# Kernel tuning notes

Hardware: AMD Instinct MI355X
Metric: run time of the kernel (lower is better)

The kernel has to match this reference:

```python
import jax, jax.numpy as jnp
import numpy as np

B, L, DIN = 2, 4096, 1024
W = 64            # windowsize
G, H = 8, 8       # groups, heads per group
DQ = DV = 64
FF = 1024
NEG = -1e30


def rmsnorm(x, gamma, d):
    # F.normalize(x, dim=-1) * sqrt(d) * gamma
    n = jnp.sqrt(jnp.sum(x * x, axis=-1, keepdims=True))
    return x / jnp.maximum(n, 1e-12) * (d ** 0.5) * gamma


def setup_inputs() -> dict:
    key = jax.random.key(0)
    ks = jax.random.split(key, 8)
    s = 0.02
    return {
        "x": jax.random.normal(ks[0], (B, L, DIN), jnp.float32),
        "norm_gamma": jnp.ones((DIN,), jnp.float32),
        "Wq_w": jax.random.normal(ks[1], (G * H * DQ, DIN), jnp.float32) * s,
        "Wq_b": jnp.zeros((G * H * DQ,), jnp.float32),
        "Wkv_w": jax.random.normal(ks[2], (G * (DQ + DV), DIN), jnp.float32) * s,
        "Wkv_b": jnp.zeros((G * (DQ + DV),), jnp.float32),
        "wz_gamma1": jnp.ones((G * H * DV,), jnp.float32),
        "W1_w": jax.random.normal(ks[3], (2 * FF, G * H * DV), jnp.float32) * s,
        "W1_b": jnp.zeros((2 * FF,), jnp.float32),
        "wz_gamma2": jnp.ones((2 * FF,), jnp.float32),
        "W2_w": jax.random.normal(ks[4], (FF, 2 * FF), jnp.float32) * s,
        "W2_b": jnp.zeros((FF,), jnp.float32),
    }


def reference(x, norm_gamma, Wq_w, Wq_b, Wkv_w, Wkv_b,
              wz_gamma1, W1_w, W1_b, wz_gamma2, W2_w, W2_b):
    w2, w4 = W // 2, W // 4
    S = 2 * L // W  # number of query chunks (L % W == 0 -> drop_last path)

    xn = rmsnorm(x, norm_gamma, DIN)
    q = xn @ Wq_w.T + Wq_b          # [B, L, G*H*DQ]
    kv = xn @ Wkv_w.T + Wkv_b       # [B, L, G*(DQ+DV)]

    # pad_to_multiple(kv, W, mod=W//2): L % W == 0 -> append W//2 zeros
    kv = jnp.pad(kv, ((0, 0), (0, w2), (0, 0)))
    k, v = jnp.split(kv, 2, axis=-1)  # each [B, L+W/2, G*DQ]
    # F.pad W//4 both sides, then overlapping windows of size W, stride W//2
    k = jnp.pad(k, ((0, 0), (w4, w4), (0, 0)))  # [B, L+W, G*DQ]
    v = jnp.pad(v, ((0, 0), (w4, w4), (0, 0)))
    idx = jnp.arange(S)[:, None] * w2 + jnp.arange(W)[None, :]  # [S, W] (drop_last applied)
    kwin = k[:, idx].reshape(B, S, W, G, DQ).transpose(0, 3, 1, 2, 4)  # [B,G,S,W,DQ]
    vwin = v[:, idx].reshape(B, S, W, G, DV).transpose(0, 3, 1, 2, 4)  # [B,G,S,W,DV]

    # 'B (S w) (G H D) -> B G H S w D'
    qh = q.reshape(B, S, w2, G, H, DQ).transpose(0, 3, 4, 1, 2, 5)  # [B,G,H,S,w2,DQ]

    qk = jnp.einsum('bghsqd,bgskd->bghsqk', qh, kwin) * (1.0 / DQ ** 0.5)
    # edge masking: first chunk can't see left pad, last chunk can't see right pad
    maskb = jnp.zeros((S, W), bool).at[0, :w4].set(True).at[S - 1, W - w4:].set(True)
    qk = jnp.where(maskb[None, None, None, :, None, :], NEG, qk)
    attn = jax.nn.softmax(qk, axis=-1)
    o = jnp.einsum('bghsqk,bgskd->bghsqd', attn, vwin)
    o = o.transpose(0, 3, 4, 1, 2, 5).reshape(B, L, G * H * DV)  # 'B G H S w D -> B (S w) (G H D)'

    # Wz: RMSNorm -> Linear -> SiLU -> RMSNorm -> Linear -> SiLU (dropout=0)
    z = rmsnorm(o, wz_gamma1, G * H * DV)
    z = jax.nn.silu(z @ W1_w.T + W1_b)
    z = rmsnorm(z, wz_gamma2, 2 * FF)
    z = jax.nn.silu(z @ W2_w.T + W2_b)
    return z
```

## Files before the change

kernel.cpp:

```cpp
#include <hip/hip_runtime.h>
#include <cstdint>

typedef _Float16 f16;
typedef f16 f16x4 __attribute__((ext_vector_type(4)));
typedef f16 f16x8 __attribute__((ext_vector_type(8)));
typedef float f32x4 __attribute__((ext_vector_type(4)));
typedef float f32x16 __attribute__((ext_vector_type(16)));

#define MFMA16(a, b, c) __builtin_amdgcn_mfma_f32_16x16x32_f16(a, b, c, 0, 0, 0)
#define MFMA32(a, b, c) __builtin_amdgcn_mfma_f32_32x32x16_f16(a, b, c, 0, 0, 0)

static __device__ __forceinline__ void gload16(const void* g, void* l) {
    __builtin_amdgcn_global_load_lds(
        (const __attribute__((address_space(1))) uint32_t*)g,
        (__attribute__((address_space(3))) uint32_t*)l, 16, 0, 0);
}

template <int NM, int ND, int NV>
static __device__ __forceinline__ void sgb_phase() {
    if (NV > 0) __builtin_amdgcn_sched_group_barrier(0x10, NV, 0);
    constexpr int PER = NM / ND;
#pragma unroll
    for (int i = 0; i < ND; ++i) {
        __builtin_amdgcn_sched_group_barrier(0x8, PER, 0);
        __builtin_amdgcn_sched_group_barrier(0x100, 1, 0);
    }
    if (NM - PER * ND > 0)
        __builtin_amdgcn_sched_group_barrier(0x8, NM - PER * ND, 0);
}

static __device__ __forceinline__ float blockReduceSum256(float v) {
    __shared__ float red[4];
#pragma unroll
    for (int off = 32; off > 0; off >>= 1) v += __shfl_xor(v, off);
    if ((threadIdx.x & 63) == 0) red[threadIdx.x >> 6] = v;
    __syncthreads();
    return red[0] + red[1] + red[2] + red[3];
}

__global__ __launch_bounds__(256) void k_rmsnorm_x(const float* __restrict__ x,
                                                   const float* __restrict__ gamma,
                                                   f16* __restrict__ out) {
    size_t row = blockIdx.x;
    const float4 v = reinterpret_cast<const float4*>(x + row * 1024)[threadIdx.x];
    float ss = v.x * v.x + v.y * v.y + v.z * v.z + v.w * v.w;
    ss = blockReduceSum256(ss);
    float sc = 32.0f / fmaxf(sqrtf(ss), 1e-12f);
    const float4 g = reinterpret_cast<const float4*>(gamma)[threadIdx.x];
    f16x4 o;
    o[0] = (f16)(v.x * sc * g.x); o[1] = (f16)(v.y * sc * g.y);
    o[2] = (f16)(v.z * sc * g.z); o[3] = (f16)(v.w * sc * g.w);
    *reinterpret_cast<f16x4*>(out + row * 1024 + threadIdx.x * 4) = o;
}

template <int D>
__global__ __launch_bounds__(256) void k_rowss(const f16* __restrict__ in,
                                               float* __restrict__ sc) {
    constexpr int PER = D / 256;
    size_t row = blockIdx.x;
    const f16* ir = in + row * D;
    int c0 = threadIdx.x * PER;
    float ss = 0.f;
#pragma unroll
    for (int i = 0; i < PER; i += 8) {
        f16x8 h = *reinterpret_cast<const f16x8*>(ir + c0 + i);
#pragma unroll
        for (int e = 0; e < 8; ++e) { float f = (float)h[e]; ss += f * f; }
    }
    ss = blockReduceSum256(ss);
    if (threadIdx.x == 0) sc[row] = ss;
}

__global__ __launch_bounds__(256) void k_prep(
    const float* __restrict__ Wq_w, const float* __restrict__ Wkv_w,
    const float* __restrict__ W1_w, const float* __restrict__ g1,
    const float* __restrict__ W2_w, const float* __restrict__ g2,
    const float* __restrict__ Wq_b, const float* __restrict__ Wkv_b,
    f16* __restrict__ wqkv, f16* __restrict__ w1, f16* __restrict__ w2,
    float* __restrict__ cb, float* __restrict__ scz) {
    int i = blockIdx.x * 256 + threadIdx.x;
    if (i < 1048576) {
        float4 v = reinterpret_cast<const float4*>(Wq_w)[i];
        f16x4 o; o[0] = (f16)v.x; o[1] = (f16)v.y; o[2] = (f16)v.z; o[3] = (f16)v.w;
        *reinterpret_cast<f16x4*>(wqkv + (size_t)i * 4) = o;
    } else if (i < 1310720) {
        int j = i - 1048576;
        float4 v = reinterpret_cast<const float4*>(Wkv_w)[j];
        f16x4 o; o[0] = (f16)v.x; o[1] = (f16)v.y; o[2] = (f16)v.z; o[3] = (f16)v.w;
        *reinterpret_cast<f16x4*>(wqkv + 4194304 + (size_t)j * 4) = o;
    } else if (i < 3407872) {
        int j = i - 1310720;
        float4 v = reinterpret_cast<const float4*>(W1_w)[j];
        int c = (j * 4) & 4095;
        f16x4 o;
        o[0] = (f16)(v.x * g1[c]);     o[1] = (f16)(v.y * g1[c + 1]);
        o[2] = (f16)(v.z * g1[c + 2]); o[3] = (f16)(v.w * g1[c + 3]);
        *reinterpret_cast<f16x4*>(w1 + (size_t)j * 4) = o;
    } else if (i < 3932160) {
        int j = i - 3407872;
        float4 v = reinterpret_cast<const float4*>(W2_w)[j];
        int c = (j * 4) & 2047;
        f16x4 o;
        o[0] = (f16)(v.x * g2[c]);     o[1] = (f16)(v.y * g2[c + 1]);
        o[2] = (f16)(v.z * g2[c + 2]); o[3] = (f16)(v.w * g2[c + 3]);
        *reinterpret_cast<f16x4*>(w2 + (size_t)j * 4) = o;
    } else if (i < 3933440) {
        int j = i - 3932160;
        int e = j * 4;
        float4 o4 = (e < 4096) ? reinterpret_cast<const float4*>(Wq_b)[j]
                               : reinterpret_cast<const float4*>(Wkv_b)[(e - 4096) >> 2];
        reinterpret_cast<float4*>(cb)[j] = o4;
    } else if (i < 3937536) {
        int j = i - 3933440;
        reinterpret_cast<float4*>(scz)[j] = make_float4(0.f, 0.f, 0.f, 0.f);
    }
}

template <int BN, int EPI>
__global__ __launch_bounds__(512, 2) void k_gemm32(const f16* __restrict__ A,
                                                   const f16* __restrict__ Bt,
                                                   const float* __restrict__ bias,
                                                   const float* __restrict__ ssin,
                                                   float sqrtD,
                                                   void* __restrict__ Cout,
                                                   int M, int N, int K) {
    constexpr int BM = 256;
    constexpr int WN = BN / 64, WM = 8 / WN;
    constexpr int WR = BM / WM, WC = BN / WN;
    constexpr int MA = WR / 32, NB = WC / 32;
    constexpr int LA = 2, LB = BN / 128;
    constexpr int VS = 2 * LA + LB;
    constexpr int AK = BM * 32, BKE = BN * 32;
    constexpr int SE = 2 * AK + 2 * BKE;

    __shared__ alignas(16) f16 lds[2 * SE];

    const int mb = M / BM;
    const int cpx = mb >> 3;
    const int xcd = blockIdx.x & 7;
    const int j = blockIdx.x >> 3;
    const int bm = xcd * cpx + (j % cpx);
    const int bn = j / cpx;

    const int tid = threadIdx.x, w = tid >> 6, l = tid & 63;
    const int wm = w / WN, wn = w % WN;
    const int cl = l & 31, h = l >> 5;

    const f16* Ab = A + (size_t)bm * BM * K;
    const f16* Bb = Bt + (size_t)bn * BN * K;
    const int NT = K >> 6;

    int aoff[MA][2], boff[NB][2];
#pragma unroll
    for (int m = 0; m < MA; ++m) {
        int r = wm * WR + m * 32 + cl;
        int gg = (r >> 1) & 3;
        aoff[m][0] = r * 32 + 8 * (h ^ gg);
        aoff[m][1] = r * 32 + 8 * ((2 | h) ^ gg);
    }
#pragma unroll
    for (int n = 0; n < NB; ++n) {
        int r = wn * WC + n * 32 + cl;
        int gg = (r >> 1) & 3;
        boff[n][0] = r * 32 + 8 * (h ^ gg);
        boff[n][1] = r * 32 + 8 * ((2 | h) ^ gg);
    }

    auto stageA = [&](int k0, f16* region) {
#pragma unroll
        for (int q = 0; q < LA; ++q) {
            int r = q * 128 + w * 16 + (l >> 2);
            int c = 8 * ((l & 3) ^ ((r >> 1) & 3));
            gload16(Ab + (size_t)r * K + k0 + c, region + q * 4096 + w * 512);
        }
    };
    auto stageB = [&](int k0, f16* region) {
#pragma unroll
        for (int q = 0; q < LB; ++q) {
            int r = q * 128 + w * 16 + (l >> 2);
            int c = 8 * ((l & 3) ^ ((r >> 1) & 3));
            gload16(Bb + (size_t)r * K + k0 + c, region + q * 4096 + w * 512);
        }
    };

    f32x16 acc[MA][NB] = {};
    f16x8 afA[MA], afB[MA], bfA[NB], bfB[NB];

    auto rdA = [&](f16x8 (&d)[MA], const f16* base, int p) {
#pragma unroll
        for (int m = 0; m < MA; ++m)
            d[m] = *reinterpret_cast<const f16x8*>(base + aoff[m][p]);
    };
    auto rdB = [&](f16x8 (&d)[NB], const f16* base, int p) {
#pragma unroll
        for (int n = 0; n < NB; ++n)
            d[n] = *reinterpret_cast<const f16x8*>(base + boff[n][p]);
    };
    auto domfma = [&](f16x8 (&af)[MA], f16x8 (&bf)[NB]) {
#pragma unroll
        for (int m = 0; m < MA; ++m)
#pragma unroll
            for (int n = 0; n < NB; ++n)
                acc[m][n] = MFMA32(af[m], bf[n], acc[m][n]);
    };

    stageA(0, lds);             stageB(0, lds + 2 * AK);
    stageA(32, lds + AK);       stageB(32, lds + 2 * AK + BKE);
    stageA(64, lds + SE);       stageB(64, lds + SE + 2 * AK);
    asm volatile("s_waitcnt vmcnt(%0)" :: "i"(2 * (LA + LB)) : "memory");
    __builtin_amdgcn_s_barrier();
    rdA(afA, lds, 0);
    rdB(bfA, lds + 2 * AK, 0);

    for (int t = 0; t < NT - 2; ++t) {
        f16* s0 = lds + (t & 1) * SE;
        f16* s1 = lds + ((t & 1) ^ 1) * SE;
        const int kn1 = (t + 1) << 6;
        const int kn2 = (t + 2) << 6;
        __builtin_amdgcn_s_barrier();
        stageA(kn1 + 32, s1 + AK);
        rdA(afB, s0, 1); rdB(bfB, s0 + 2 * AK, 1);
        domfma(afA, bfA);
        sgb_phase<MA * NB, MA + NB, LA>();
        asm volatile("s_waitcnt vmcnt(%0)" :: "i"(VS) : "memory");
        __builtin_amdgcn_s_barrier();
        stageB(kn1 + 32, s1 + 2 * AK + BKE);
        rdA(afA, s0 + AK, 0); rdB(bfA, s0 + 2 * AK + BKE, 0);
        domfma(afB, bfB);
        sgb_phase<MA * NB, MA + NB, LB>();
        __builtin_amdgcn_s_barrier();
        stageA(kn2, s0);
        rdA(afB, s0 + AK, 1); rdB(bfB, s0 + 2 * AK + BKE, 1);
        domfma(afA, bfA);
        sgb_phase<MA * NB, MA + NB, LA>();
        asm volatile("s_waitcnt vmcnt(%0)" :: "i"(VS) : "memory");
        __builtin_amdgcn_s_barrier();
        stageB(kn2, s0 + 2 * AK);
        rdA(afA, s1, 0); rdB(bfA, s1 + 2 * AK, 0);
        domfma(afB, bfB);
        sgb_phase<MA * NB, MA + NB, LB>();
    }
    {
        const int t = NT - 2;
        f16* s0 = lds + (t & 1) * SE;
        f16* s1 = lds + ((t & 1) ^ 1) * SE;
        const int kn1 = (t + 1) << 6;
        __builtin_amdgcn_s_barrier();
        stageA(kn1 + 32, s1 + AK);
        rdA(afB, s0, 1); rdB(bfB, s0 + 2 * AK, 1);
        domfma(afA, bfA);
        sgb_phase<MA * NB, MA + NB, LA>();
        asm volatile("s_waitcnt vmcnt(%0)" :: "i"(VS) : "memory");
        __builtin_amdgcn_s_barrier();
        stageB(kn1 + 32, s1 + 2 * AK + BKE);
        rdA(afA, s0 + AK, 0); rdB(bfA, s0 + 2 * AK + BKE, 0);
        domfma(afB, bfB);
        sgb_phase<MA * NB, MA + NB, LB>();
        __builtin_amdgcn_s_barrier();
        rdA(afB, s0 + AK, 1); rdB(bfB, s0 + 2 * AK + BKE, 1);
        domfma(afA, bfA);
        sgb_phase<MA * NB, MA + NB, 0>();
        asm volatile("s_waitcnt vmcnt(%0)" :: "i"(LA + LB) : "memory");
        __builtin_amdgcn_s_barrier();
        rdA(afA, s1, 0); rdB(bfA, s1 + 2 * AK, 0);
        domfma(afB, bfB);
        sgb_phase<MA * NB, MA + NB, 0>();
    }
    {
        f16* s0 = lds + ((NT - 1) & 1) * SE;
        __builtin_amdgcn_s_barrier();
        rdA(afB, s0, 1); rdB(bfB, s0 + 2 * AK, 1);
        domfma(afA, bfA);
        sgb_phase<MA * NB, MA + NB, 0>();
        asm volatile("s_waitcnt vmcnt(0)" ::: "memory");
        __builtin_amdgcn_s_barrier();
        rdA(afA, s0 + AK, 0); rdB(bfA, s0 + 2 * AK + BKE, 0);
        domfma(afB, bfB);
        sgb_phase<MA * NB, MA + NB, 0>();
        rdA(afB, s0 + AK, 1); rdB(bfB, s0 + 2 * AK + BKE, 1);
        domfma(afA, bfA);
        sgb_phase<MA * NB, MA + NB, 0>();
        domfma(afB, bfB);
    }

    const size_t row0 = (size_t)bm * BM + wm * WR;
    const int col0 = bn * BN + wn * WC;
    float bsv[NB];
#pragma unroll
    for (int n = 0; n < NB; ++n) bsv[n] = bias[col0 + n * 32 + cl];
#pragma unroll
    for (int m = 0; m < MA; ++m) {
#pragma unroll
        for (int jr = 0; jr < 16; ++jr) {
            const size_t row = row0 + m * 32 + h * 4 + (jr & 3) + 8 * (jr >> 2);
            float scl = 1.0f;
            if (EPI >= 1) scl = sqrtD * rsqrtf(fmaxf(ssin[row], 1e-24f));
#pragma unroll
            for (int n = 0; n < NB; ++n) {
                float v = acc[m][n][jr];
                if (EPI >= 1) v = v * scl;
                v += bsv[n];
                if (EPI >= 1) v = v / (1.f + __expf(-v));
                const size_t idx = row * (size_t)N + col0 + n * 32 + cl;
                if (EPI == 2) reinterpret_cast<float*>(Cout)[idx] = v;
                else          reinterpret_cast<f16*>(Cout)[idx] = (f16)v;
            }
        }
    }
}

__global__ __launch_bounds__(256) void k_attn(const f16* __restrict__ qkv,
                                              f16* __restrict__ o,
                                              float* __restrict__ ssout) {
    __shared__ alignas(16) f16 Ksm[64 * 64];
    __shared__ alignas(16) f16 Vtsm[64 * 64];
    __shared__ alignas(16) f16 Psm[4][64 * 64];
    const int idx = blockIdx.x;
    const int s = idx & 127;
    const int g = (idx >> 7) & 7;
    const int b = idx >> 10;
    const int tid = threadIdx.x;
    const int w = tid >> 6, l = tid & 63;

    const int baseR = s * 32 - 16;
#pragma unroll
    for (int i = 0; i < 2; ++i) {
        const int j = i * 32 + (tid >> 3);
        const int d0 = (tid & 7) * 8;
        const int R = baseR + j;
        f16x8 kvv = {}, vvv = {};
        if (R >= 0 && R < 4096) {
            const f16* rp = qkv + ((size_t)(b * 4096 + R)) * 5120 + 4096 + g * 64 + d0;
            kvv = *reinterpret_cast<const f16x8*>(rp);
            vvv = *reinterpret_cast<const f16x8*>(rp + 512);
        }
        *reinterpret_cast<f16x8*>(&Ksm[j * 64 + d0]) = kvv;
#pragma unroll
        for (int e = 0; e < 8; ++e) Vtsm[(d0 + e) * 64 + j] = vvv[e];
    }

    const int lrow = l & 15, lk = (l >> 4) * 8;
    f16x8 aq[4][2];
#pragma unroll
    for (int m = 0; m < 4; ++m) {
        const int qr = w * 64 + m * 16 + lrow;
        const int h = qr >> 5, qi = qr & 31;
        const f16* qp = qkv + ((size_t)(b * 4096 + s * 32 + qi)) * 5120 + (g * 8 + h) * 64 + lk;
        aq[m][0] = *reinterpret_cast<const f16x8*>(qp);
        aq[m][1] = *reinterpret_cast<const f16x8*>(qp + 32);
    }
    __syncthreads();

    f32x4 acc[4][4] = {};
#pragma unroll
    for (int kk = 0; kk < 2; ++kk) {
        f16x8 bk[4];
#pragma unroll
        for (int n = 0; n < 4; ++n)
            bk[n] = *reinterpret_cast<const f16x8*>(&Ksm[(n * 16 + lrow) * 64 + kk * 32 + lk]);
#pragma unroll
        for (int m = 0; m < 4; ++m)
#pragma unroll
            for (int n = 0; n < 4; ++n)
                acc[m][n] = MFMA16(aq[m][kk], bk[n], acc[m][n]);
    }

    const int nlo = (s == 0) ? 1 : 0;
    const int nhi = (s == 127) ? 3 : 4;
#pragma unroll
    for (int m = 0; m < 4; ++m) {
#pragma unroll
        for (int r = 0; r < 4; ++r) {
            float xv[4];
#pragma unroll
            for (int n = 0; n < 4; ++n) xv[n] = acc[m][n][r] * 0.125f;
            float mx = -1e30f;
            for (int n = nlo; n < nhi; ++n) mx = fmaxf(mx, xv[n]);
#pragma unroll
            for (int off = 8; off > 0; off >>= 1) mx = fmaxf(mx, __shfl_xor(mx, off));
            float pv[4]; float sum = 0.f;
#pragma unroll
            for (int n = 0; n < 4; ++n) {
                float e = (n >= nlo && n < nhi) ? __expf(xv[n] - mx) : 0.f;
                pv[n] = e; sum += e;
            }
#pragma unroll
            for (int off = 8; off > 0; off >>= 1) sum += __shfl_xor(sum, off);
            const float inv = 1.f / sum;
            const int prow = m * 16 + (l >> 4) * 4 + r;
#pragma unroll
            for (int n = 0; n < 4; ++n)
                Psm[w][prow * 64 + n * 16 + lrow] = (f16)(pv[n] * inv);
        }
    }
    __syncthreads();

    f32x4 oacc[4][4] = {};
#pragma unroll
    for (int kk = 0; kk < 2; ++kk) {
        f16x8 ap[4], bv[4];
#pragma unroll
        for (int m = 0; m < 4; ++m)
            ap[m] = *reinterpret_cast<const f16x8*>(&Psm[w][(m * 16 + lrow) * 64 + kk * 32 + lk]);
#pragma unroll
        for (int n = 0; n < 4; ++n)
            bv[n] = *reinterpret_cast<const f16x8*>(&Vtsm[(n * 16 + lrow) * 64 + kk * 32 + lk]);
#pragma unroll
        for (int m = 0; m < 4; ++m)
#pragma unroll
            for (int n = 0; n < 4; ++n)
                oacc[m][n] = MFMA16(ap[m], bv[n], oacc[m][n]);
    }
    const int lr4 = (l >> 4) * 4;
#pragma unroll
    for (int m = 0; m < 4; ++m) {
#pragma unroll
        for (int r = 0; r < 4; ++r) {
            const int qr = w * 64 + m * 16 + lr4 + r;
            const int h = qr >> 5, qi = qr & 31;
            f16* op = o + ((size_t)(b * 4096 + s * 32 + qi)) * 4096 + (g * 8 + h) * 64;
            float ssp = 0.f;
#pragma unroll
            for (int n = 0; n < 4; ++n) {
                float v = oacc[m][n][r];
                op[n * 16 + lrow] = (f16)v;
                ssp += v * v;
            }
            ssp += __shfl_xor(ssp, 1);
            ssp += __shfl_xor(ssp, 2);
            ssp += __shfl_xor(ssp, 4);
            ssp += __shfl_xor(ssp, 8);
            if (lrow == 0)
                atomicAdd(&ssout[(size_t)(b * 4096 + s * 32 + qi)], ssp);
        }
    }
}

extern "C" void kernel_launch(void* const* d_in, const int* in_sizes, int n_in,
                              void* d_out, int out_size, void* d_ws, size_t ws_size,
                              hipStream_t stream) {
    const float* x     = (const float*)d_in[0];
    const float* ng    = (const float*)d_in[1];
    const float* Wq_w  = (const float*)d_in[2];
    const float* Wq_b  = (const float*)d_in[3];
    const float* Wkv_w = (const float*)d_in[4];
    const float* Wkv_b = (const float*)d_in[5];
    const float* g1    = (const float*)d_in[6];
    const float* W1_w  = (const float*)d_in[7];
    const float* W1_b  = (const float*)d_in[8];
    const float* g2    = (const float*)d_in[9];
    const float* W2_w  = (const float*)d_in[10];
    const float* W2_b  = (const float*)d_in[11];
    float* out = (float*)d_out;

    char* p = (char*)d_ws;
    f16* qkv  = (f16*)(p);
    f16* h1   = (f16*)(p);
    f16* xn   = (f16*)(p + 83886080);
    f16* ob   = (f16*)(p + 83886080);
    f16* w1   = (f16*)(p + 150994944);
    f16* w2   = (f16*)(p + 167772160);
    f16* wqkv = (f16*)(p + 171966464);
    float* cb  = (float*)(p + 182452224);
    float* sc1 = (float*)(p + 182472704);
    float* sc2 = (float*)(p + 182505472);

    k_prep<<<15381, 256, 0, stream>>>(Wq_w, Wkv_w, W1_w, g1, W2_w, g2, Wq_b, Wkv_b,
                                      wqkv, w1, w2, cb, sc1);
    k_rmsnorm_x<<<8192, 256, 0, stream>>>(x, ng, xn);

    k_gemm32<256, 0><<<640, 512, 0, stream>>>(xn, wqkv, cb, nullptr, 0.f,
                                              qkv, 8192, 5120, 1024);

    k_attn<<<2048, 256, 0, stream>>>(qkv, ob, sc1);

    k_gemm32<256, 1><<<256, 512, 0, stream>>>(ob, w1, W1_b, sc1, 64.0f,
                                              h1, 8192, 2048, 4096);
    k_rowss<2048><<<8192, 256, 0, stream>>>(h1, sc2);
    k_gemm32<128, 2><<<256, 512, 0, stream>>>(h1, w2, W2_b, sc2, 45.254834f,
                                              (void*)out, 8192, 1024, 2048);

    (void)in_sizes; (void)n_in; (void)out_size; (void)ws_size;
}
```

Before: 366.7 us.

## Drop redundant GEMM pipeline barriers, change LDS swizzle, fold input rmsnorm into prep

```diff
diff --git a/kernel.cpp b/kernel.cpp
--- a/kernel.cpp
+++ b/kernel.cpp
@@ -22,7 +22,7 @@
     constexpr int PER = NM / ND;
 #pragma unroll
     for (int i = 0; i < ND; ++i) {
-        __builtin_amdgcn_sched_group_barrier(0x8, PER, 0);
+        if (PER > 0) __builtin_amdgcn_sched_group_barrier(0x8, PER, 0);
         __builtin_amdgcn_sched_group_barrier(0x100, 1, 0);
     }
     if (NM - PER * ND > 0)
@@ -36,21 +36,6 @@
     if ((threadIdx.x & 63) == 0) red[threadIdx.x >> 6] = v;
     __syncthreads();
     return red[0] + red[1] + red[2] + red[3];
-}
-
-__global__ __launch_bounds__(256) void k_rmsnorm_x(const float* __restrict__ x,
-                                                   const float* __restrict__ gamma,
-                                                   f16* __restrict__ out) {
-    size_t row = blockIdx.x;
-    const float4 v = reinterpret_cast<const float4*>(x + row * 1024)[threadIdx.x];
-    float ss = v.x * v.x + v.y * v.y + v.z * v.z + v.w * v.w;
-    ss = blockReduceSum256(ss);
-    float sc = 32.0f / fmaxf(sqrtf(ss), 1e-12f);
-    const float4 g = reinterpret_cast<const float4*>(gamma)[threadIdx.x];
-    f16x4 o;
-    o[0] = (f16)(v.x * sc * g.x); o[1] = (f16)(v.y * sc * g.y);
-    o[2] = (f16)(v.z * sc * g.z); o[3] = (f16)(v.w * sc * g.w);
-    *reinterpret_cast<f16x4*>(out + row * 1024 + threadIdx.x * 4) = o;
 }
 
 template <int D>
@@ -72,13 +57,27 @@
 }
 
 __global__ __launch_bounds__(256) void k_prep(
+    const float* __restrict__ x, const float* __restrict__ ng, f16* __restrict__ xn,
     const float* __restrict__ Wq_w, const float* __restrict__ Wkv_w,
     const float* __restrict__ W1_w, const float* __restrict__ g1,
     const float* __restrict__ W2_w, const float* __restrict__ g2,
     const float* __restrict__ Wq_b, const float* __restrict__ Wkv_b,
     f16* __restrict__ wqkv, f16* __restrict__ w1, f16* __restrict__ w2,
     float* __restrict__ cb, float* __restrict__ scz) {
-    int i = blockIdx.x * 256 + threadIdx.x;
+    if (blockIdx.x < 8192) {
+        size_t row = blockIdx.x;
+        const float4 v = reinterpret_cast<const float4*>(x + row * 1024)[threadIdx.x];
+        float ss = v.x * v.x + v.y * v.y + v.z * v.z + v.w * v.w;
+        ss = blockReduceSum256(ss);
+        float sc = 32.0f / fmaxf(sqrtf(ss), 1e-12f);
+        const float4 g = reinterpret_cast<const float4*>(ng)[threadIdx.x];
+        f16x4 o;
+        o[0] = (f16)(v.x * sc * g.x); o[1] = (f16)(v.y * sc * g.y);
+        o[2] = (f16)(v.z * sc * g.z); o[3] = (f16)(v.w * sc * g.w);
+        *reinterpret_cast<f16x4*>(xn + row * 1024 + threadIdx.x * 4) = o;
+        return;
+    }
+    int i = (blockIdx.x - 8192) * 256 + threadIdx.x;
     if (i < 1048576) {
         float4 v = reinterpret_cast<const float4*>(Wq_w)[i];
         f16x4 o; o[0] = (f16)v.x; o[1] = (f16)v.y; o[2] = (f16)v.z; o[3] = (f16)v.w;
@@ -116,7 +115,11 @@
     }
 }
 
-template <int BN, int EPI>
+static __device__ __forceinline__ int swz4(int r) {
+    return ((r >> 1) ^ (r >> 3)) & 3;
+}
+
+template <int BM, int BN, int EPI>
 __global__ __launch_bounds__(512, 2) void k_gemm32(const f16* __restrict__ A,
                                                    const f16* __restrict__ Bt,
                                                    const float* __restrict__ bias,
@@ -124,13 +127,12 @@
                                                    float sqrtD,
                                                    void* __restrict__ Cout,
                                                    int M, int N, int K) {
-    constexpr int BM = 256;
-    constexpr int WN = BN / 64, WM = 8 / WN;
-    constexpr int WR = BM / WM, WC = BN / WN;
-    constexpr int MA = WR / 32, NB = WC / 32;
-    constexpr int LA = 2, LB = BN / 128;
+    constexpr int WN = BN / 64, WM = 8 / WN, WR = BM / WM;
+    constexpr int MA = WR / 32, NB = 2;
+    constexpr int LA = BM / 128, LB = BN / 128;
     constexpr int VS = 2 * LA + LB;
-    constexpr int AK = BM * 32, BKE = BN * 32;
+    constexpr int AK = BM * 32;
+    constexpr int BKE = BN * 32;
     constexpr int SE = 2 * AK + 2 * BKE;
 
     __shared__ alignas(16) f16 lds[2 * SE];
@@ -154,14 +156,14 @@
 #pragma unroll
     for (int m = 0; m < MA; ++m) {
         int r = wm * WR + m * 32 + cl;
-        int gg = (r >> 1) & 3;
+        int gg = swz4(r);
         aoff[m][0] = r * 32 + 8 * (h ^ gg);
         aoff[m][1] = r * 32 + 8 * ((2 | h) ^ gg);
     }
 #pragma unroll
     for (int n = 0; n < NB; ++n) {
-        int r = wn * WC + n * 32 + cl;
-        int gg = (r >> 1) & 3;
+        int r = wn * 64 + n * 32 + cl;
+        int gg = swz4(r);
         boff[n][0] = r * 32 + 8 * (h ^ gg);
         boff[n][1] = r * 32 + 8 * ((2 | h) ^ gg);
     }
@@ -170,7 +172,7 @@
 #pragma unroll
         for (int q = 0; q < LA; ++q) {
             int r = q * 128 + w * 16 + (l >> 2);
-            int c = 8 * ((l & 3) ^ ((r >> 1) & 3));
+            int c = 8 * ((l & 3) ^ swz4(r));
             gload16(Ab + (size_t)r * K + k0 + c, region + q * 4096 + w * 512);
         }
     };
@@ -178,14 +180,10 @@
 #pragma unroll
         for (int q = 0; q < LB; ++q) {
             int r = q * 128 + w * 16 + (l >> 2);
-            int c = 8 * ((l & 3) ^ ((r >> 1) & 3));
+            int c = 8 * ((l & 3) ^ swz4(r));
             gload16(Bb + (size_t)r * K + k0 + c, region + q * 4096 + w * 512);
         }
     };
-
-    f32x16 acc[MA][NB] = {};
-    f16x8 afA[MA], afB[MA], bfA[NB], bfB[NB];
-
     auto rdA = [&](f16x8 (&d)[MA], const f16* base, int p) {
 #pragma unroll
         for (int m = 0; m < MA; ++m)
@@ -196,6 +194,10 @@
         for (int n = 0; n < NB; ++n)
             d[n] = *reinterpret_cast<const f16x8*>(base + boff[n][p]);
     };
+
+    f32x16 acc[MA][NB] = {};
+    f16x8 afA[MA], afB[MA], bfA[NB], bfB[NB];
+
     auto domfma = [&](f16x8 (&af)[MA], f16x8 (&bf)[NB]) {
 #pragma unroll
         for (int m = 0; m < MA; ++m)
@@ -212,12 +214,12 @@
     rdA(afA, lds, 0);
     rdB(bfA, lds + 2 * AK, 0);
 
-    for (int t = 0; t < NT - 2; ++t) {
+    const int NTm2 = NT - 2;
+    for (int t = 0; t < NTm2; ++t) {
         f16* s0 = lds + (t & 1) * SE;
         f16* s1 = lds + ((t & 1) ^ 1) * SE;
         const int kn1 = (t + 1) << 6;
         const int kn2 = (t + 2) << 6;
-        __builtin_amdgcn_s_barrier();
         stageA(kn1 + 32, s1 + AK);
         rdA(afB, s0, 1); rdB(bfB, s0 + 2 * AK, 1);
         domfma(afA, bfA);
@@ -228,7 +230,6 @@
         rdA(afA, s0 + AK, 0); rdB(bfA, s0 + 2 * AK + BKE, 0);
         domfma(afB, bfB);
         sgb_phase<MA * NB, MA + NB, LB>();
-        __builtin_amdgcn_s_barrier();
         stageA(kn2, s0);
         rdA(afB, s0 + AK, 1); rdB(bfB, s0 + 2 * AK + BKE, 1);
         domfma(afA, bfA);
@@ -241,11 +242,10 @@
         sgb_phase<MA * NB, MA + NB, LB>();
     }
     {
-        const int t = NT - 2;
+        const int t = NTm2;
         f16* s0 = lds + (t & 1) * SE;
         f16* s1 = lds + ((t & 1) ^ 1) * SE;
         const int kn1 = (t + 1) << 6;
-        __builtin_amdgcn_s_barrier();
         stageA(kn1 + 32, s1 + AK);
         rdA(afB, s0, 1); rdB(bfB, s0 + 2 * AK, 1);
         domfma(afA, bfA);
@@ -256,7 +256,6 @@
         rdA(afA, s0 + AK, 0); rdB(bfA, s0 + 2 * AK + BKE, 0);
         domfma(afB, bfB);
         sgb_phase<MA * NB, MA + NB, LB>();
-        __builtin_amdgcn_s_barrier();
         rdA(afB, s0 + AK, 1); rdB(bfB, s0 + 2 * AK + BKE, 1);
         domfma(afA, bfA);
         sgb_phase<MA * NB, MA + NB, 0>();
@@ -268,7 +267,6 @@
     }
     {
         f16* s0 = lds + ((NT - 1) & 1) * SE;
-        __builtin_amdgcn_s_barrier();
         rdA(afB, s0, 1); rdB(bfB, s0 + 2 * AK, 1);
         domfma(afA, bfA);
         sgb_phase<MA * NB, MA + NB, 0>();
@@ -284,7 +282,7 @@
     }
 
     const size_t row0 = (size_t)bm * BM + wm * WR;
-    const int col0 = bn * BN + wn * WC;
+    const int col0 = bn * BN + wn * 64;
     float bsv[NB];
 #pragma unroll
     for (int n = 0; n < NB; ++n) bsv[n] = bias[col0 + n * 32 + cl];
@@ -465,20 +463,20 @@
     float* sc1 = (float*)(p + 182472704);
     float* sc2 = (float*)(p + 182505472);
 
-    k_prep<<<15381, 256, 0, stream>>>(Wq_w, Wkv_w, W1_w, g1, W2_w, g2, Wq_b, Wkv_b,
-                                      wqkv, w1, w2, cb, sc1);
-    k_rmsnorm_x<<<8192, 256, 0, stream>>>(x, ng, xn);
-
-    k_gemm32<256, 0><<<640, 512, 0, stream>>>(xn, wqkv, cb, nullptr, 0.f,
-                                              qkv, 8192, 5120, 1024);
+    k_prep<<<8192 + 15381, 256, 0, stream>>>(x, ng, xn,
+                                             Wq_w, Wkv_w, W1_w, g1, W2_w, g2,
+                                             Wq_b, Wkv_b, wqkv, w1, w2, cb, sc1);
+
+    k_gemm32<256, 256, 0><<<640, 512, 0, stream>>>(xn, wqkv, cb, nullptr, 0.f,
+                                                   qkv, 8192, 5120, 1024);
 
     k_attn<<<2048, 256, 0, stream>>>(qkv, ob, sc1);
 
-    k_gemm32<256, 1><<<256, 512, 0, stream>>>(ob, w1, W1_b, sc1, 64.0f,
-                                              h1, 8192, 2048, 4096);
+    k_gemm32<256, 256, 1><<<256, 512, 0, stream>>>(ob, w1, W1_b, sc1, 64.0f,
+                                                   h1, 8192, 2048, 4096);
     k_rowss<2048><<<8192, 256, 0, stream>>>(h1, sc2);
-    k_gemm32<128, 2><<<256, 512, 0, stream>>>(h1, w2, W2_b, sc2, 45.254834f,
-                                              (void*)out, 8192, 1024, 2048);
+    k_gemm32<256, 128, 2><<<256, 512, 0, stream>>>(h1, w2, W2_b, sc2, 45.254834f,
+                                                   (void*)out, 8192, 1024, 2048);
 
     (void)in_sizes; (void)n_in; (void)out_size; (void)ws_size;
 }
```

Result: no change. 360.5 us (-1.7%).
